# Kernel optimization log

Hardware: AMD Instinct MI355X
Metric: run time of the kernel (lower is better)

The kernel has to match this reference:

```python
import jax, jax.numpy as jnp
import numpy as np

T, B, D_IN, H = 512, 256, 64, 128


def _normc(key, shape):
    w = jax.random.normal(key, shape, dtype=jnp.float32)
    return w / jnp.sqrt(jnp.sum(w * w, axis=1, keepdims=True))


def setup_inputs() -> dict:
    key = jax.random.key(0)
    ks = jax.random.split(key, 8)
    state = jax.random.normal(ks[0], (T, B, D_IN), dtype=jnp.float32)
    # PyTorch LSTMCell params: weight_ih [4H, in], weight_hh [4H, H], biases [4H]
    s = 1.0 / np.sqrt(H)
    W_ih0 = jax.random.uniform(ks[1], (4 * H, D_IN), minval=-s, maxval=s, dtype=jnp.float32)
    W_hh0 = jax.random.uniform(ks[2], (4 * H, H), minval=-s, maxval=s, dtype=jnp.float32)
    b_ih0 = jnp.zeros((4 * H,), jnp.float32)
    b_hh0 = jnp.zeros((4 * H,), jnp.float32)
    W_ih1 = jax.random.uniform(ks[3], (4 * H, H), minval=-s, maxval=s, dtype=jnp.float32)
    W_hh1 = jax.random.uniform(ks[4], (4 * H, H), minval=-s, maxval=s, dtype=jnp.float32)
    b_ih1 = jnp.zeros((4 * H,), jnp.float32)
    b_hh1 = jnp.zeros((4 * H,), jnp.float32)
    # normc-initialized output head (rows normalized to unit norm, zero bias)
    W_out = _normc(ks[5], (1, H))
    b_out = jnp.zeros((1,), jnp.float32)
    return dict(state=state, W_ih0=W_ih0, W_hh0=W_hh0, b_ih0=b_ih0, b_hh0=b_hh0,
                W_ih1=W_ih1, W_hh1=W_hh1, b_ih1=b_ih1, b_hh1=b_hh1,
                W_out=W_out, b_out=b_out)


def _lstm_cell(x, h, c, W_ih, W_hh, b_ih, b_hh):
    # gates: [B, 4H], chunk order i, f, g, o (PyTorch convention)
    g = x @ W_ih.T + b_ih + h @ W_hh.T + b_hh
    i, f, gg, o = jnp.split(g, 4, axis=-1)
    i = jax.nn.sigmoid(i)
    f = jax.nn.sigmoid(f)
    gg = jnp.tanh(gg)
    o = jax.nn.sigmoid(o)
    c2 = f * c + i * gg
    h2 = o * jnp.tanh(c2)
    return h2, c2


def reference(state, W_ih0, W_hh0, b_ih0, b_hh0, W_ih1, W_hh1, b_ih1, b_hh1, W_out, b_out):
    Bsz = state.shape[1]
    Hd = W_hh0.shape[1]
    z = jnp.zeros((Bsz, Hd), state.dtype)

    def step(carry, x_t):
        h0, c0, h1, c1 = carry
        h0, c0 = _lstm_cell(x_t, h0, c0, W_ih0, W_hh0, b_ih0, b_hh0)
        h1, c1 = _lstm_cell(h0, h1, c1, W_ih1, W_hh1, b_ih1, b_hh1)
        v_t = h1 @ W_out.T + b_out  # [B, 1]
        return (h0, c0, h1, c1), v_t

    _, values = jax.lax.scan(step, (z, z, z, z), state)
    return values  # [T, B, 1]
```

## Files before the change

kernel.cpp:

```cpp
#include <hip/hip_runtime.h>


#define T_STEPS 512
#define BATCH   256
#define DIN     64
#define GROUP   16
#define NGRP    (T_STEPS / GROUP)

typedef _Float16 half8 __attribute__((ext_vector_type(8)));
typedef _Float16 half4 __attribute__((ext_vector_type(4)));
typedef float    f32x4 __attribute__((ext_vector_type(4)));

#define LOG2E  1.44269504088896f
#define LOG2E2 2.88539008177793f

#define WH_IH0 0
#define WH_HH0 32768
#define WH_IH1 98304
#define WH_HH1 163840
#define WH_X2     229376
#define WH_SLAB2  8617984
#define WB_FLAG2  50790400
#define WS2_TOTAL 50823168
#define WH_SLAB1  229376
#define WB_FLAG1  34013184
#define WS1_TOTAL 34045952
#define WS0XH_TOTAL ((size_t)(WH_X2 + 8388608) * 2)

__global__ void prep_weights(const float* __restrict__ wih0,
                             const float* __restrict__ whh0,
                             const float* __restrict__ wih1,
                             const float* __restrict__ whh1,
                             _Float16* __restrict__ ws) {
    int idx = blockIdx.x * 256 + threadIdx.x;
    float v; int row;
    if (idx < 32768)       { row = idx >> 6;             v = wih0[idx]; }
    else if (idx < 98304)  { row = (idx - 32768) >> 7;   v = whh0[idx - 32768]; }
    else if (idx < 163840) { row = (idx - 98304) >> 7;   v = wih1[idx - 98304]; }
    else                   { row = (idx - 163840) >> 7;  v = whh1[idx - 163840]; }
    float sc = ((row >> 7) == 2) ? LOG2E2 : LOG2E;
    ws[idx] = (_Float16)(v * sc);
}

__global__ void prep_state(const float* __restrict__ s, _Float16* __restrict__ d) {
    int i = (blockIdx.x * 256 + threadIdx.x) * 8;
    f32x4 a = *(const f32x4*)(s + i);
    f32x4 b = *(const f32x4*)(s + i + 4);
    half8 h;
    h[0]=(_Float16)a[0]; h[1]=(_Float16)a[1]; h[2]=(_Float16)a[2]; h[3]=(_Float16)a[3];
    h[4]=(_Float16)b[0]; h[5]=(_Float16)b[1]; h[6]=(_Float16)b[2]; h[7]=(_Float16)b[3];
    *(half8*)(d + i) = h;
}

__device__ __forceinline__ float rcpf(float x) { return __builtin_amdgcn_rcpf(x); }
__device__ __forceinline__ float ex2(float x)  { return __builtin_amdgcn_exp2f(x); }

__device__ __forceinline__ float sig2(float y) {
    return rcpf(1.0f + ex2(-y));
}
__device__ __forceinline__ float tanh2(float y2) {
    return 1.0f - 2.0f * rcpf(1.0f + ex2(y2));
}
__device__ __forceinline__ float tanh_c(float c) {
    return 1.0f - 2.0f * rcpf(1.0f + ex2(c * LOG2E2));
}

__device__ __forceinline__ float act_row(float aI, float aF, float aG, float aO,
                                         float& ccv) {
    float Ei = ex2(-aI);
    float Ef = ex2(-aF);
    float Eg = ex2(aG);
    float Eo = ex2(-aO);
    float fg  = rcpf(1.0f + Ef);
    float igg = (Eg - 1.0f) * rcpf((1.0f + Ei) * (1.0f + Eg));
    float c   = fg * ccv + igg;
    ccv = c;
    float Ec = ex2(c * LOG2E2);
    return (Ec - 1.0f) * rcpf((1.0f + Eo) * (1.0f + Ec));
}

#define PIPE_LDS_BYTES ((4096 + 128) * 2)

template<bool XH>
__global__ __launch_bounds__(512, 1) void lstm_pipe(
        const float* __restrict__ state32, const _Float16* __restrict__ wsw,
        const float* __restrict__ b_ih0, const float* __restrict__ b_hh0,
        const float* __restrict__ b_ih1, const float* __restrict__ b_hh1,
        const float* __restrict__ w_out, const float* __restrict__ b_out,
        _Float16* __restrict__ slab, int* __restrict__ flags,
        const _Float16* __restrict__ xh, float* __restrict__ out) {
    extern __shared__ _Float16 lds[];
    _Float16* hdb   = lds;
    _Float16* woutl = lds + 4096;

    const int tid  = threadIdx.x;
    const int w    = tid >> 6;
    const int lane = tid & 63;
    const int col  = lane & 15;
    const int quad = lane >> 4;
    const bool producer = blockIdx.x < 16;
    const int tile = blockIdx.x & 15;
    const int rowbase = tile * 16;
    const int j0 = w * 16 + col;

    {
        half8 z;
        #pragma unroll
        for (int jj = 0; jj < 8; ++jj) z[jj] = (_Float16)0.0f;
        *(half8*)(hdb + tid * 8) = z;
    }
    if (!producer && tid < 128) woutl[tid] = (_Float16)w_out[tid];

    half8 wresf[4][4];
    float bias[4];
    #pragma unroll
    for (int nt = 0; nt < 4; ++nt) {
        int j = nt * 128 + j0;
        float sc = (nt == 2) ? LOG2E2 : LOG2E;
        if (producer) {
            #pragma unroll
            for (int kt = 0; kt < 2; ++kt)
                wresf[nt][kt] = *(const half8*)(wsw + WH_IH0 + j * 64 + kt * 32 + quad * 8);
            bias[nt] = (b_ih0[j] + b_hh0[j]) * sc;
        } else {
            #pragma unroll
            for (int kt = 0; kt < 4; ++kt)
                wresf[nt][kt] = *(const half8*)(wsw + WH_IH1 + j * 128 + kt * 32 + quad * 8);
            bias[nt] = (b_ih1[j] + b_hh1[j]) * sc;
        }
    }
    const float bout = b_out[0];

    half8 wpf[4][4];
    {
        const _Float16* wrg = wsw + (producer ? WH_HH0 : WH_HH1);
        #pragma unroll
        for (int kt = 0; kt < 4; ++kt)
            #pragma unroll
            for (int nt = 0; nt < 4; ++nt)
                wpf[kt][nt] = *(const half8*)(wrg + (nt * 128 + j0) * 128 + kt * 32 + quad * 8);
    }
    #pragma unroll
    for (int kt = 0; kt < 4; ++kt)
        #pragma unroll
        for (int nt = 0; nt < 4; ++nt)
            asm volatile("" : "+v"(wpf[kt][nt]));

    int swz[4], hoff[4], w0off[4];
    #pragma unroll
    for (int kt = 0; kt < 4; ++kt) {
        swz[kt]  = ((kt * 4 + quad) ^ col) * 8;
        hoff[kt] = col * 128 + swz[kt];
    }
    #pragma unroll
    for (int i = 0; i < 4; ++i) {
        int row = quad * 4 + i;
        w0off[i] = row * 128 + (((2 * w + (col >> 3)) ^ row) * 8) + (col & 7);
    }
    float cc[4] = {0.f, 0.f, 0.f, 0.f};

    const int cr   = tid >> 5;
    const int cc0  = (tid & 31) * 4;
    const int cprd = cr * 128 + (((cc0 >> 3) ^ cr) * 8) + (cc0 & 7);

    __syncthreads();

    if (producer) {
        const _Float16* xph = xh + (size_t)(rowbase + col) * DIN + quad * 8;
        const float*    xpf = state32 + (size_t)(rowbase + col) * DIN + quad * 8;

        half8 bx0, bx1;
        f32x4 bf0, bf1, bf2, bf3;
        f32x4 accI[4];
        {
            half8 a0, a1v;
            if constexpr (XH) {
                a0  = *(const half8*)(xph);
                a1v = *(const half8*)(xph + 32);
            } else {
                f32x4 t0 = *(const f32x4*)(xpf),      t1 = *(const f32x4*)(xpf + 4);
                f32x4 t2 = *(const f32x4*)(xpf + 32), t3 = *(const f32x4*)(xpf + 36);
                #pragma unroll
                for (int jj = 0; jj < 4; ++jj) {
                    a0[jj]  = (_Float16)t0[jj]; a0[jj+4]  = (_Float16)t1[jj];
                    a1v[jj] = (_Float16)t2[jj]; a1v[jj+4] = (_Float16)t3[jj];
                }
            }
            #pragma unroll
            for (int nt = 0; nt < 4; ++nt) {
                f32x4 b = {bias[nt], bias[nt], bias[nt], bias[nt]};
                accI[nt] = b;
            }
            #pragma unroll
            for (int nt = 0; nt < 4; ++nt)
                accI[nt] = __builtin_amdgcn_mfma_f32_16x16x32_f16(a0, wresf[nt][0], accI[nt], 0, 0, 0);
            #pragma unroll
            for (int nt = 0; nt < 4; ++nt)
                accI[nt] = __builtin_amdgcn_mfma_f32_16x16x32_f16(a1v, wresf[nt][1], accI[nt], 0, 0, 0);
            if constexpr (XH) {
                bx0 = *(const half8*)(xph + BATCH * DIN);
                bx1 = *(const half8*)(xph + BATCH * DIN + 32);
            } else {
                bf0 = *(const f32x4*)(xpf + BATCH * DIN);
                bf1 = *(const f32x4*)(xpf + BATCH * DIN + 4);
                bf2 = *(const f32x4*)(xpf + BATCH * DIN + 32);
                bf3 = *(const f32x4*)(xpf + BATCH * DIN + 36);
            }
        }

        #pragma unroll 2
        for (int t = 0; t < T_STEPS; ++t) {
            const int pbo = (t & 1) * 2048, cbo = pbo ^ 2048;
            const int lt = t & (GROUP - 1);
            __syncthreads();

            if (t > 0) {
                half4 hv = *(const half4*)(hdb + pbo + cprd);
                *(half4*)(slab + (size_t)((t - 1) * 16 + tile) * 2048 + tid * 4) = hv;
            }
            if (lt == 1 && t > 16 && tid == 0)
                __hip_atomic_store(flags + ((t >> 4) - 1) * 16 + tile, t >> 4,
                                   __ATOMIC_RELEASE, __HIP_MEMORY_SCOPE_AGENT);

            half8 ah[4];
            #pragma unroll
            for (int kt = 0; kt < 4; ++kt)
                ah[kt] = *(const half8*)(hdb + pbo + hoff[kt]);

            #pragma unroll
            for (int kt = 0; kt < 4; ++kt)
                #pragma unroll
                for (int nt = 0; nt < 4; ++nt)
                    accI[nt] = __builtin_amdgcn_mfma_f32_16x16x32_f16(ah[kt], wpf[kt][nt], accI[nt], 0, 0, 0);

            half8 fx0, fx1;
            f32x4 ff0, ff1, ff2, ff3;
            {
                int tn2 = (t + 2 < T_STEPS) ? t + 2 : T_STEPS - 1;
                if constexpr (XH) {
                    const _Float16* xq = xph + (size_t)tn2 * (BATCH * DIN);
                    fx0 = *(const half8*)(xq);
                    fx1 = *(const half8*)(xq + 32);
                } else {
                    const float* xq = xpf + (size_t)tn2 * (BATCH * DIN);
                    ff0 = *(const f32x4*)(xq);      ff1 = *(const f32x4*)(xq + 4);
                    ff2 = *(const f32x4*)(xq + 32); ff3 = *(const f32x4*)(xq + 36);
                }
            }

            half8 cx0, cx1;
            if constexpr (XH) { cx0 = bx0; cx1 = bx1; }
            else {
                #pragma unroll
                for (int jj = 0; jj < 4; ++jj) {
                    cx0[jj] = (_Float16)bf0[jj]; cx0[jj+4] = (_Float16)bf1[jj];
                    cx1[jj] = (_Float16)bf2[jj]; cx1[jj+4] = (_Float16)bf3[jj];
                }
            }
            f32x4 accN[4];
            #pragma unroll
            for (int nt = 0; nt < 4; ++nt) {
                f32x4 b = {bias[nt], bias[nt], bias[nt], bias[nt]};
                accN[nt] = b;
            }
            #pragma unroll
            for (int i = 0; i < 4; ++i) {
                if (i < 2) {
                    half8 cxk = (i == 0) ? cx0 : cx1;
                    #pragma unroll
                    for (int nt = 0; nt < 4; ++nt)
                        accN[nt] = __builtin_amdgcn_mfma_f32_16x16x32_f16(cxk, wresf[nt][i], accN[nt], 0, 0, 0);
                    __builtin_amdgcn_sched_group_barrier(0x008, 4, 0);
                }
                float hval = act_row(accI[0][i], accI[1][i], accI[2][i], accI[3][i], cc[i]);
                hdb[cbo + w0off[i]] = (_Float16)hval;
                __builtin_amdgcn_sched_group_barrier(0x002, 16, 0);
            }

            #pragma unroll
            for (int nt = 0; nt < 4; ++nt) accI[nt] = accN[nt];
            if constexpr (XH) { bx0 = fx0; bx1 = fx1; }
            else { bf0 = ff0; bf1 = ff1; bf2 = ff2; bf3 = ff3; }
        }
        __syncthreads();
        {
            half4 hv = *(const half4*)(hdb + 0 + cprd);
            *(half4*)(slab + (size_t)((T_STEPS - 1) * 16 + tile) * 2048 + tid * 4) = hv;
        }
        __syncthreads();
        if (tid == 0)
            __hip_atomic_store(flags + (NGRP - 1) * 16 + tile, NGRP,
                               __ATOMIC_RELEASE, __HIP_MEMORY_SCOPE_AGENT);
    } else {
        if (tid == 0) {
            while (__hip_atomic_load(flags + tile, __ATOMIC_ACQUIRE,
                                     __HIP_MEMORY_SCOPE_AGENT) < 1)
                __builtin_amdgcn_s_sleep(1);
        }
        __syncthreads();

        half8 uA[4];
        f32x4 accI[4];
        {
            const _Float16* s0 = slab + (size_t)tile * 2048;
            half8 cA[4];
            #pragma unroll
            for (int kt = 0; kt < 4; ++kt)
                cA[kt] = *(const half8*)(s0 + col * 128 + kt * 32 + quad * 8);
            #pragma unroll
            for (int nt = 0; nt < 4; ++nt) {
                f32x4 b = {bias[nt], bias[nt], bias[nt], bias[nt]};
                accI[nt] = b;
            }
            #pragma unroll
            for (int kt = 0; kt < 4; ++kt)
                #pragma unroll
                for (int nt = 0; nt < 4; ++nt)
                    accI[nt] = __builtin_amdgcn_mfma_f32_16x16x32_f16(cA[kt], wresf[nt][kt], accI[nt], 0, 0, 0);
            const _Float16* s1 = slab + (size_t)(16 + tile) * 2048;
            #pragma unroll
            for (int kt = 0; kt < 4; ++kt)
                uA[kt] = *(const half8*)(s1 + col * 128 + kt * 32 + quad * 8);
        }

        #pragma unroll 2
        for (int t = 0; t < T_STEPS; ++t) {
            const int pbo = (t & 1) * 2048, cbo = pbo ^ 2048;
            const int lt = t & (GROUP - 1);
            __syncthreads();

            half8 a1[4];
            #pragma unroll
            for (int kt = 0; kt < 4; ++kt)
                a1[kt] = *(const half8*)(hdb + pbo + hoff[kt]);

            #pragma unroll
            for (int kt = 0; kt < 4; ++kt)
                #pragma unroll
                for (int nt = 0; nt < 4; ++nt)
                    accI[nt] = __builtin_amdgcn_mfma_f32_16x16x32_f16(a1[kt], wpf[kt][nt], accI[nt], 0, 0, 0);

            if (lt == 12 && tid == 0) {
                int g1 = (t >> 4) + 1;
                if (g1 < NGRP) {
                    while (__hip_atomic_load(flags + g1 * 16 + tile, __ATOMIC_ACQUIRE,
                                             __HIP_MEMORY_SCOPE_AGENT) < g1 + 1)
                        __builtin_amdgcn_s_sleep(1);
                }
            }

            half8 fA[4];
            {
                int tn2 = (t + 2 < T_STEPS) ? t + 2 : T_STEPS - 1;
                const _Float16* sq = slab + (size_t)(tn2 * 16 + tile) * 2048;
                #pragma unroll
                for (int kt = 0; kt < 4; ++kt)
                    fA[kt] = *(const half8*)(sq + col * 128 + kt * 32 + quad * 8);
            }

            f32x4 accN[4];
            #pragma unroll
            for (int nt = 0; nt < 4; ++nt) {
                f32x4 b = {bias[nt], bias[nt], bias[nt], bias[nt]};
                accN[nt] = b;
            }
            #pragma unroll
            for (int i = 0; i < 4; ++i) {
                #pragma unroll
                for (int nt = 0; nt < 4; ++nt)
                    accN[nt] = __builtin_amdgcn_mfma_f32_16x16x32_f16(uA[i], wresf[nt][i], accN[nt], 0, 0, 0);
                __builtin_amdgcn_sched_group_barrier(0x008, 4, 0);
                float hval = act_row(accI[0][i], accI[1][i], accI[2][i], accI[3][i], cc[i]);
                hdb[cbo + w0off[i]] = (_Float16)hval;
                __builtin_amdgcn_sched_group_barrier(0x002, 16, 0);
            }

            if (w == 7) {
                f32x4 vh = {0.f, 0.f, 0.f, 0.f};
                #pragma unroll
                for (int kt = 0; kt < 4; ++kt) {
                    half8 av = *(const half8*)(hdb + pbo + hoff[kt]);
                    half8 bw = *(const half8*)(woutl + kt * 32 + quad * 8);
                    vh = __builtin_amdgcn_mfma_f32_16x16x32_f16(av, bw, vh, 0, 0, 0);
                }
                if (t > 0 && col == 0) {
                    f32x4 vo = {vh[0] + bout, vh[1] + bout, vh[2] + bout, vh[3] + bout};
                    *(f32x4*)(out + (size_t)(t - 1) * BATCH + rowbase + quad * 4) = vo;
                }
            }

            #pragma unroll
            for (int nt = 0; nt < 4; ++nt) accI[nt] = accN[nt];
            #pragma unroll
            for (int kt = 0; kt < 4; ++kt) uA[kt] = fA[kt];
        }
        __syncthreads();
        if (w == 7) {
            const int fbo = (((T_STEPS - 1) & 1) ^ 1) * 2048;
            f32x4 vh = {0.f, 0.f, 0.f, 0.f};
            #pragma unroll
            for (int kt = 0; kt < 4; ++kt) {
                half8 av = *(const half8*)(hdb + fbo + hoff[kt]);
                half8 bw = *(const half8*)(woutl + kt * 32 + quad * 8);
                vh = __builtin_amdgcn_mfma_f32_16x16x32_f16(av, bw, vh, 0, 0, 0);
            }
            if (col == 0) {
                f32x4 vo = {vh[0] + bout, vh[1] + bout, vh[2] + bout, vh[3] + bout};
                *(f32x4*)(out + (size_t)(T_STEPS - 1) * BATCH + rowbase + quad * 4) = vo;
            }
        }
    }
}

#define MONO_LDS_BYTES ((73728 + 128) * 2)

template<bool XH>
__global__ __launch_bounds__(512, 2) void lstm_mono(
        const float* __restrict__ state32, const _Float16* __restrict__ wsw,
        const float* __restrict__ b_ih0, const float* __restrict__ b_hh0,
        const float* __restrict__ b_ih1, const float* __restrict__ b_hh1,
        const float* __restrict__ w_out, const float* __restrict__ b_out,
        float* __restrict__ out) {
    extern __shared__ _Float16 lds[];
    _Float16* whh1  = lds;
    _Float16* h0b   = lds + 65536;
    _Float16* h1b   = lds + 69632;
    _Float16* woutl = lds + 73728;

    const int tid  = threadIdx.x;
    const int w    = tid >> 6;
    const int lane = tid & 63;
    const int col  = lane & 15;
    const int quad = lane >> 4;
    const int rowbase = blockIdx.x * 16;
    const int j0 = w * 16 + col;

    const _Float16* whh1g = wsw + WH_HH1;
    #pragma unroll
    for (int it = 0; it < 16; ++it) {
        int flat = (it * 512 + tid) * 8;
        int r = flat >> 7, chunk = (flat >> 3) & 15;
        *(half8*)(whh1 + r * 128 + ((chunk ^ (r & 15)) * 8)) = *(const half8*)(whh1g + flat);
    }
    {
        half8 z;
        #pragma unroll
        for (int jj = 0; jj < 8; ++jj) z[jj] = (_Float16)0.0f;
        for (int i = tid * 8; i < 8192; i += 4096) *(half8*)(h0b + i) = z;
    }
    if (tid < 128) woutl[tid] = (_Float16)w_out[tid];

    half8 whh0f[4][4], wih1f[4][4];
    float bias0[4], bias1[4];
    #pragma unroll
    for (int nt = 0; nt < 4; ++nt) {
        int j = nt * 128 + j0;
        float sc = (nt == 2) ? LOG2E2 : LOG2E;
        #pragma unroll
        for (int kt = 0; kt < 4; ++kt) {
            whh0f[nt][kt] = *(const half8*)(wsw + WH_HH0 + j * 128 + kt * 32 + quad * 8);
            wih1f[nt][kt] = *(const half8*)(wsw + WH_IH1 + j * 128 + kt * 32 + quad * 8);
        }
        bias0[nt] = (b_ih0[j] + b_hh0[j]) * sc;
        bias1[nt] = (b_ih1[j] + b_hh1[j]) * sc;
    }
    const float bout = b_out[0];

    int swz[4], hoff[4], w0off[4];
    #pragma unroll
    for (int kt = 0; kt < 4; ++kt) {
        swz[kt]  = ((kt * 4 + quad) ^ col) * 8;
        hoff[kt] = col * 128 + swz[kt];
    }
    #pragma unroll
    for (int i = 0; i < 4; ++i) {
        int row = quad * 4 + i;
        w0off[i] = row * 128 + (((2 * w + (col >> 3)) ^ row) * 8) + (col & 7);
    }
    float c0[4] = {0.f,0.f,0.f,0.f}, c1[4] = {0.f,0.f,0.f,0.f};

    const _Float16* xph = wsw + WH_X2 + (size_t)(rowbase + col) * DIN + quad * 8;
    const float*    xpf = state32 + (size_t)(rowbase + col) * DIN + quad * 8;
    half8 nxh0, nxh1;
    f32x4 nxf0, nxf1, nxf2, nxf3;
    if constexpr (XH) {
        nxh0 = *(const half8*)(xph); nxh1 = *(const half8*)(xph + 32);
    } else {
        nxf0 = *(const f32x4*)(xpf);      nxf1 = *(const f32x4*)(xpf + 4);
        nxf2 = *(const f32x4*)(xpf + 32); nxf3 = *(const f32x4*)(xpf + 36);
    }
    __syncthreads();
    const _Float16* wih0g = wsw + WH_IH0;

    #pragma unroll 1
    for (int t = 0; t < T_STEPS; ++t) {
        const int pbo = (t & 1) * 2048, cbo = pbo ^ 2048;
        half8 ax0, ax1;
        if constexpr (XH) { ax0 = nxh0; ax1 = nxh1; }
        else {
            #pragma unroll
            for (int jj = 0; jj < 4; ++jj) {
                ax0[jj]   = (_Float16)nxf0[jj]; ax0[jj+4] = (_Float16)nxf1[jj];
                ax1[jj]   = (_Float16)nxf2[jj]; ax1[jj+4] = (_Float16)nxf3[jj];
            }
        }
        half8 wif[4][2];
        #pragma unroll
        for (int nt = 0; nt < 4; ++nt)
            #pragma unroll
            for (int kt = 0; kt < 2; ++kt)
                wif[nt][kt] = *(const half8*)(wih0g + (nt * 128 + j0) * 64 + kt * 32 + quad * 8);
        half8 ah[4];
        #pragma unroll
        for (int kt = 0; kt < 4; ++kt)
            ah[kt] = *(const half8*)(h0b + pbo + hoff[kt]);

        f32x4 acc[4];
        #pragma unroll
        for (int nt = 0; nt < 4; ++nt) {
            f32x4 b = {bias0[nt], bias0[nt], bias0[nt], bias0[nt]};
            acc[nt] = b;
        }
        #pragma unroll
        for (int kt = 0; kt < 4; ++kt)
            #pragma unroll
            for (int nt = 0; nt < 4; ++nt)
                acc[nt] = __builtin_amdgcn_mfma_f32_16x16x32_f16(ah[kt], whh0f[nt][kt], acc[nt], 0, 0, 0);
        #pragma unroll
        for (int kt = 0; kt < 2; ++kt) {
            half8 axk = kt ? ax1 : ax0;
            #pragma unroll
            for (int nt = 0; nt < 4; ++nt)
                acc[nt] = __builtin_amdgcn_mfma_f32_16x16x32_f16(axk, wif[nt][kt], acc[nt], 0, 0, 0);
        }
        {
            int tn = (t + 1 < T_STEPS) ? t + 1 : t;
            if constexpr (XH) {
                const _Float16* xq = xph + (size_t)tn * (BATCH * DIN);
                nxh0 = *(const half8*)(xq); nxh1 = *(const half8*)(xq + 32);
            } else {
                const float* xq = xpf + (size_t)tn * (BATCH * DIN);
                nxf0 = *(const f32x4*)(xq);      nxf1 = *(const f32x4*)(xq + 4);
                nxf2 = *(const f32x4*)(xq + 32); nxf3 = *(const f32x4*)(xq + 36);
            }
        }
        #pragma unroll
        for (int i = 0; i < 4; ++i) {
            float ig = sig2(acc[0][i]);
            float fg = sig2(acc[1][i]);
            float gg = tanh2(acc[2][i]);
            float og = sig2(acc[3][i]);
            float c  = fg * c0[i] + ig * gg;
            c0[i] = c;
            h0b[cbo + w0off[i]] = (_Float16)(og * tanh_c(c));
        }
        __syncthreads();

        #pragma unroll
        for (int nt = 0; nt < 4; ++nt) {
            f32x4 b = {bias1[nt], bias1[nt], bias1[nt], bias1[nt]};
            acc[nt] = b;
        }
        #pragma unroll
        for (int kt = 0; kt < 4; ++kt) {
            half8 a0 = *(const half8*)(h0b + cbo + hoff[kt]);
            half8 a1 = *(const half8*)(h1b + pbo + hoff[kt]);
            #pragma unroll
            for (int nt = 0; nt < 4; ++nt)
                acc[nt] = __builtin_amdgcn_mfma_f32_16x16x32_f16(a0, wih1f[nt][kt], acc[nt], 0, 0, 0);
            #pragma unroll
            for (int nt = 0; nt < 4; ++nt) {
                half8 bfr = *(const half8*)(whh1 + nt * 16384 + j0 * 128 + swz[kt]);
                acc[nt] = __builtin_amdgcn_mfma_f32_16x16x32_f16(a1, bfr, acc[nt], 0, 0, 0);
            }
        }
        #pragma unroll
        for (int i = 0; i < 4; ++i) {
            float ig = sig2(acc[0][i]);
            float fg = sig2(acc[1][i]);
            float gg = tanh2(acc[2][i]);
            float og = sig2(acc[3][i]);
            float c  = fg * c1[i] + ig * gg;
            c1[i] = c;
            h1b[cbo + w0off[i]] = (_Float16)(og * tanh_c(c));
        }
        if (w == 7) {
            f32x4 vh = {0.f, 0.f, 0.f, 0.f};
            #pragma unroll
            for (int kt = 0; kt < 4; ++kt) {
                half8 a1 = *(const half8*)(h1b + pbo + hoff[kt]);
                half8 bw = *(const half8*)(woutl + kt * 32 + quad * 8);
                vh = __builtin_amdgcn_mfma_f32_16x16x32_f16(a1, bw, vh, 0, 0, 0);
            }
            if (t > 0 && col == 0) {
                f32x4 vo = {vh[0] + bout, vh[1] + bout, vh[2] + bout, vh[3] + bout};
                *(f32x4*)(out + (size_t)(t - 1) * BATCH + rowbase + quad * 4) = vo;
            }
        }
    }
    __syncthreads();
    if (w == 7) {
        const int fbo = (((T_STEPS - 1) & 1) ^ 1) * 2048;
        f32x4 vh = {0.f, 0.f, 0.f, 0.f};
        #pragma unroll
        for (int kt = 0; kt < 4; ++kt) {
            half8 a1 = *(const half8*)(h1b + fbo + hoff[kt]);
            half8 bw = *(const half8*)(woutl + kt * 32 + quad * 8);
            vh = __builtin_amdgcn_mfma_f32_16x16x32_f16(a1, bw, vh, 0, 0, 0);
        }
        if (col == 0) {
            f32x4 vo = {vh[0] + bout, vh[1] + bout, vh[2] + bout, vh[3] + bout};
            *(f32x4*)(out + (size_t)(T_STEPS - 1) * BATCH + rowbase + quad * 4) = vo;
        }
    }
}

extern "C" void kernel_launch(void* const* d_in, const int* in_sizes, int n_in,
                              void* d_out, int out_size, void* d_ws, size_t ws_size,
                              hipStream_t stream) {
    const float* state = (const float*)d_in[0];
    const float* wih0  = (const float*)d_in[1];
    const float* whh0  = (const float*)d_in[2];
    const float* bih0  = (const float*)d_in[3];
    const float* bhh0  = (const float*)d_in[4];
    const float* wih1  = (const float*)d_in[5];
    const float* whh1  = (const float*)d_in[6];
    const float* bih1  = (const float*)d_in[7];
    const float* bhh1  = (const float*)d_in[8];
    const float* wout  = (const float*)d_in[9];
    const float* bout  = (const float*)d_in[10];
    _Float16* wsh = (_Float16*)d_ws;
    float* outp = (float*)d_out;

    prep_weights<<<896, 256, 0, stream>>>(wih0, whh0, wih1, whh1, wsh);

    if (ws_size >= WS2_TOTAL) {
        prep_state<<<4096, 256, 0, stream>>>(state, wsh + WH_X2);
        lstm_pipe<true><<<32, 512, PIPE_LDS_BYTES, stream>>>(
            state, wsh, bih0, bhh0, bih1, bhh1, wout, bout,
            wsh + WH_SLAB2, (int*)((char*)d_ws + WB_FLAG2), wsh + WH_X2, outp);
    } else if (ws_size >= WS1_TOTAL) {
        lstm_pipe<false><<<32, 512, PIPE_LDS_BYTES, stream>>>(
            state, wsh, bih0, bhh0, bih1, bhh1, wout, bout,
            wsh + WH_SLAB1, (int*)((char*)d_ws + WB_FLAG1), nullptr, outp);
    } else if (ws_size >= WS0XH_TOTAL) {
        prep_state<<<4096, 256, 0, stream>>>(state, wsh + WH_X2);
        lstm_mono<true><<<16, 512, MONO_LDS_BYTES, stream>>>(
            state, wsh, bih0, bhh0, bih1, bhh1, wout, bout, outp);
    } else {
        lstm_mono<false><<<16, 512, MONO_LDS_BYTES, stream>>>(
            state, wsh, bih0, bhh0, bih1, bhh1, wout, bout, outp);
    }
}
```

Measured before the change: 608.7 us.

## Drop fp16 state pre-conversion pass and fold bias into first MFMA

Removes the separate prep_state kernel and the fp16 copy of the input sequence, so the pipelined LSTM always reads fp32 state and converts it in-register. This skips an extra kernel launch and a full pass over the 32 MB input, at the cost of twice the bytes read per step inside the recurrent loop. Bias is now passed as the accumulator operand of the first MFMA instead of being splatted separately. The explicit sched_group_barrier interleaving of MFMA and activation code is also removed, leaving instruction scheduling to the compiler.

```diff
diff --git a/kernel.cpp b/kernel.cpp
--- a/kernel.cpp
+++ b/kernel.cpp
@@ -18,14 +18,9 @@
 #define WH_HH0 32768
 #define WH_IH1 98304
 #define WH_HH1 163840
-#define WH_X2     229376
-#define WH_SLAB2  8617984
-#define WB_FLAG2  50790400
-#define WS2_TOTAL 50823168
 #define WH_SLAB1  229376
 #define WB_FLAG1  34013184
 #define WS1_TOTAL 34045952
-#define WS0XH_TOTAL ((size_t)(WH_X2 + 8388608) * 2)
 
 __global__ void prep_weights(const float* __restrict__ wih0,
                              const float* __restrict__ whh0,
@@ -42,28 +37,12 @@
     ws[idx] = (_Float16)(v * sc);
 }
 
-__global__ void prep_state(const float* __restrict__ s, _Float16* __restrict__ d) {
-    int i = (blockIdx.x * 256 + threadIdx.x) * 8;
-    f32x4 a = *(const f32x4*)(s + i);
-    f32x4 b = *(const f32x4*)(s + i + 4);
-    half8 h;
-    h[0]=(_Float16)a[0]; h[1]=(_Float16)a[1]; h[2]=(_Float16)a[2]; h[3]=(_Float16)a[3];
-    h[4]=(_Float16)b[0]; h[5]=(_Float16)b[1]; h[6]=(_Float16)b[2]; h[7]=(_Float16)b[3];
-    *(half8*)(d + i) = h;
-}
-
 __device__ __forceinline__ float rcpf(float x) { return __builtin_amdgcn_rcpf(x); }
 __device__ __forceinline__ float ex2(float x)  { return __builtin_amdgcn_exp2f(x); }
 
-__device__ __forceinline__ float sig2(float y) {
-    return rcpf(1.0f + ex2(-y));
-}
-__device__ __forceinline__ float tanh2(float y2) {
-    return 1.0f - 2.0f * rcpf(1.0f + ex2(y2));
-}
-__device__ __forceinline__ float tanh_c(float c) {
-    return 1.0f - 2.0f * rcpf(1.0f + ex2(c * LOG2E2));
-}
+__device__ __forceinline__ float sig2(float y)  { return rcpf(1.0f + ex2(-y)); }
+__device__ __forceinline__ float tanh2(float y2){ return 1.0f - 2.0f * rcpf(1.0f + ex2(y2)); }
+__device__ __forceinline__ float tanh_c(float c){ return 1.0f - 2.0f * rcpf(1.0f + ex2(c * LOG2E2)); }
 
 __device__ __forceinline__ float act_row(float aI, float aF, float aG, float aO,
                                          float& ccv) {
@@ -81,14 +60,13 @@
 
 #define PIPE_LDS_BYTES ((4096 + 128) * 2)
 
-template<bool XH>
 __global__ __launch_bounds__(512, 1) void lstm_pipe(
         const float* __restrict__ state32, const _Float16* __restrict__ wsw,
         const float* __restrict__ b_ih0, const float* __restrict__ b_hh0,
         const float* __restrict__ b_ih1, const float* __restrict__ b_hh1,
         const float* __restrict__ w_out, const float* __restrict__ b_out,
         _Float16* __restrict__ slab, int* __restrict__ flags,
-        const _Float16* __restrict__ xh, float* __restrict__ out) {
+        float* __restrict__ out) {
     extern __shared__ _Float16 lds[];
     _Float16* hdb   = lds;
     _Float16* woutl = lds + 4096;
@@ -112,22 +90,25 @@
     if (!producer && tid < 128) woutl[tid] = (_Float16)w_out[tid];
 
     half8 wresf[4][4];
-    float bias[4];
+    f32x4 biasv[4];
     #pragma unroll
     for (int nt = 0; nt < 4; ++nt) {
         int j = nt * 128 + j0;
         float sc = (nt == 2) ? LOG2E2 : LOG2E;
+        float b;
         if (producer) {
             #pragma unroll
             for (int kt = 0; kt < 2; ++kt)
                 wresf[nt][kt] = *(const half8*)(wsw + WH_IH0 + j * 64 + kt * 32 + quad * 8);
-            bias[nt] = (b_ih0[j] + b_hh0[j]) * sc;
+            b = (b_ih0[j] + b_hh0[j]) * sc;
         } else {
             #pragma unroll
             for (int kt = 0; kt < 4; ++kt)
                 wresf[nt][kt] = *(const half8*)(wsw + WH_IH1 + j * 128 + kt * 32 + quad * 8);
-            bias[nt] = (b_ih1[j] + b_hh1[j]) * sc;
-        }
+            b = (b_ih1[j] + b_hh1[j]) * sc;
+        }
+        f32x4 bv = {b, b, b, b};
+        biasv[nt] = bv;
     }
     const float bout = b_out[0];
 
@@ -166,46 +147,29 @@
     __syncthreads();
 
     if (producer) {
-        const _Float16* xph = xh + (size_t)(rowbase + col) * DIN + quad * 8;
-        const float*    xpf = state32 + (size_t)(rowbase + col) * DIN + quad * 8;
-
-        half8 bx0, bx1;
+        const float* xpf = state32 + (size_t)(rowbase + col) * DIN + quad * 8;
+
         f32x4 bf0, bf1, bf2, bf3;
         f32x4 accI[4];
         {
+            f32x4 t0 = *(const f32x4*)(xpf),      t1 = *(const f32x4*)(xpf + 4);
+            f32x4 t2 = *(const f32x4*)(xpf + 32), t3 = *(const f32x4*)(xpf + 36);
             half8 a0, a1v;
-            if constexpr (XH) {
-                a0  = *(const half8*)(xph);
-                a1v = *(const half8*)(xph + 32);
-            } else {
-                f32x4 t0 = *(const f32x4*)(xpf),      t1 = *(const f32x4*)(xpf + 4);
-                f32x4 t2 = *(const f32x4*)(xpf + 32), t3 = *(const f32x4*)(xpf + 36);
-                #pragma unroll
-                for (int jj = 0; jj < 4; ++jj) {
-                    a0[jj]  = (_Float16)t0[jj]; a0[jj+4]  = (_Float16)t1[jj];
-                    a1v[jj] = (_Float16)t2[jj]; a1v[jj+4] = (_Float16)t3[jj];
-                }
-            }
-            #pragma unroll
-            for (int nt = 0; nt < 4; ++nt) {
-                f32x4 b = {bias[nt], bias[nt], bias[nt], bias[nt]};
-                accI[nt] = b;
-            }
-            #pragma unroll
-            for (int nt = 0; nt < 4; ++nt)
-                accI[nt] = __builtin_amdgcn_mfma_f32_16x16x32_f16(a0, wresf[nt][0], accI[nt], 0, 0, 0);
+            #pragma unroll
+            for (int jj = 0; jj < 4; ++jj) {
+                a0[jj]  = (_Float16)t0[jj]; a0[jj+4]  = (_Float16)t1[jj];
+                a1v[jj] = (_Float16)t2[jj]; a1v[jj+4] = (_Float16)t3[jj];
+            }
+            #pragma unroll
+            for (int nt = 0; nt < 4; ++nt)
+                accI[nt] = __builtin_amdgcn_mfma_f32_16x16x32_f16(a0, wresf[nt][0], biasv[nt], 0, 0, 0);
             #pragma unroll
             for (int nt = 0; nt < 4; ++nt)
                 accI[nt] = __builtin_amdgcn_mfma_f32_16x16x32_f16(a1v, wresf[nt][1], accI[nt], 0, 0, 0);
-            if constexpr (XH) {
-                bx0 = *(const half8*)(xph + BATCH * DIN);
-                bx1 = *(const half8*)(xph + BATCH * DIN + 32);
-            } else {
-                bf0 = *(const f32x4*)(xpf + BATCH * DIN);
-                bf1 = *(const f32x4*)(xpf + BATCH * DIN + 4);
-                bf2 = *(const f32x4*)(xpf + BATCH * DIN + 32);
-                bf3 = *(const f32x4*)(xpf + BATCH * DIN + 36);
-            }
+            bf0 = *(const f32x4*)(xpf + BATCH * DIN);
+            bf1 = *(const f32x4*)(xpf + BATCH * DIN + 4);
+            bf2 = *(const f32x4*)(xpf + BATCH * DIN + 32);
+            bf3 = *(const f32x4*)(xpf + BATCH * DIN + 36);
         }
 
         #pragma unroll 2
@@ -233,54 +197,37 @@
                 for (int nt = 0; nt < 4; ++nt)
                     accI[nt] = __builtin_amdgcn_mfma_f32_16x16x32_f16(ah[kt], wpf[kt][nt], accI[nt], 0, 0, 0);
 
-            half8 fx0, fx1;
             f32x4 ff0, ff1, ff2, ff3;
             {
                 int tn2 = (t + 2 < T_STEPS) ? t + 2 : T_STEPS - 1;
-                if constexpr (XH) {
-                    const _Float16* xq = xph + (size_t)tn2 * (BATCH * DIN);
-                    fx0 = *(const half8*)(xq);
-                    fx1 = *(const half8*)(xq + 32);
-                } else {
-                    const float* xq = xpf + (size_t)tn2 * (BATCH * DIN);
-                    ff0 = *(const f32x4*)(xq);      ff1 = *(const f32x4*)(xq + 4);
-                    ff2 = *(const f32x4*)(xq + 32); ff3 = *(const f32x4*)(xq + 36);
-                }
+                const float* xq = xpf + (size_t)tn2 * (BATCH * DIN);
+                ff0 = *(const f32x4*)(xq);      ff1 = *(const f32x4*)(xq + 4);
+                ff2 = *(const f32x4*)(xq + 32); ff3 = *(const f32x4*)(xq + 36);
             }
 
             half8 cx0, cx1;
-            if constexpr (XH) { cx0 = bx0; cx1 = bx1; }
-            else {
-                #pragma unroll
-                for (int jj = 0; jj < 4; ++jj) {
-                    cx0[jj] = (_Float16)bf0[jj]; cx0[jj+4] = (_Float16)bf1[jj];
-                    cx1[jj] = (_Float16)bf2[jj]; cx1[jj+4] = (_Float16)bf3[jj];
-                }
+            #pragma unroll
+            for (int jj = 0; jj < 4; ++jj) {
+                cx0[jj] = (_Float16)bf0[jj]; cx0[jj+4] = (_Float16)bf1[jj];
+                cx1[jj] = (_Float16)bf2[jj]; cx1[jj+4] = (_Float16)bf3[jj];
             }
             f32x4 accN[4];
             #pragma unroll
-            for (int nt = 0; nt < 4; ++nt) {
-                f32x4 b = {bias[nt], bias[nt], bias[nt], bias[nt]};
-                accN[nt] = b;
-            }
+            for (int nt = 0; nt < 4; ++nt)
+                accN[nt] = __builtin_amdgcn_mfma_f32_16x16x32_f16(cx0, wresf[nt][0], biasv[nt], 0, 0, 0);
+            #pragma unroll
+            for (int nt = 0; nt < 4; ++nt)
+                accN[nt] = __builtin_amdgcn_mfma_f32_16x16x32_f16(cx1, wresf[nt][1], accN[nt], 0, 0, 0);
+
             #pragma unroll
             for (int i = 0; i < 4; ++i) {
-                if (i < 2) {
-                    half8 cxk = (i == 0) ? cx0 : cx1;
-                    #pragma unroll
-                    for (int nt = 0; nt < 4; ++nt)
-                        accN[nt] = __builtin_amdgcn_mfma_f32_16x16x32_f16(cxk, wresf[nt][i], accN[nt], 0, 0, 0);
-                    __builtin_amdgcn_sched_group_barrier(0x008, 4, 0);
-                }
                 float hval = act_row(accI[0][i], accI[1][i], accI[2][i], accI[3][i], cc[i]);
                 hdb[cbo + w0off[i]] = (_Float16)hval;
-                __builtin_amdgcn_sched_group_barrier(0x002, 16, 0);
             }
 
             #pragma unroll
             for (int nt = 0; nt < 4; ++nt) accI[nt] = accN[nt];
-            if constexpr (XH) { bx0 = fx0; bx1 = fx1; }
-            else { bf0 = ff0; bf1 = ff1; bf2 = ff2; bf3 = ff3; }
+            bf0 = ff0; bf1 = ff1; bf2 = ff2; bf3 = ff3;
         }
         __syncthreads();
         {
@@ -308,12 +255,10 @@
             for (int kt = 0; kt < 4; ++kt)
                 cA[kt] = *(const half8*)(s0 + col * 128 + kt * 32 + quad * 8);
             #pragma unroll
-            for (int nt = 0; nt < 4; ++nt) {
-                f32x4 b = {bias[nt], bias[nt], bias[nt], bias[nt]};
-                accI[nt] = b;
-            }
-            #pragma unroll
-            for (int kt = 0; kt < 4; ++kt)
+            for (int nt = 0; nt < 4; ++nt)
+                accI[nt] = __builtin_amdgcn_mfma_f32_16x16x32_f16(cA[0], wresf[nt][0], biasv[nt], 0, 0, 0);
+            #pragma unroll
+            for (int kt = 1; kt < 4; ++kt)
                 #pragma unroll
                 for (int nt = 0; nt < 4; ++nt)
                     accI[nt] = __builtin_amdgcn_mfma_f32_16x16x32_f16(cA[kt], wresf[nt][kt], accI[nt], 0, 0, 0);
@@ -360,19 +305,18 @@
 
             f32x4 accN[4];
             #pragma unroll
-            for (int nt = 0; nt < 4; ++nt) {
-                f32x4 b = {bias[nt], bias[nt], bias[nt], bias[nt]};
-                accN[nt] = b;
-            }
-            #pragma unroll
-            for (int i = 0; i < 4; ++i) {
+            for (int nt = 0; nt < 4; ++nt)
+                accN[nt] = __builtin_amdgcn_mfma_f32_16x16x32_f16(uA[0], wresf[nt][0], biasv[nt], 0, 0, 0);
+            #pragma unroll
+            for (int kt = 1; kt < 4; ++kt)
                 #pragma unroll
                 for (int nt = 0; nt < 4; ++nt)
-                    accN[nt] = __builtin_amdgcn_mfma_f32_16x16x32_f16(uA[i], wresf[nt][i], accN[nt], 0, 0, 0);
-                __builtin_amdgcn_sched_group_barrier(0x008, 4, 0);
+                    accN[nt] = __builtin_amdgcn_mfma_f32_16x16x32_f16(uA[kt], wresf[nt][kt], accN[nt], 0, 0, 0);
+
+            #pragma unroll
+            for (int i = 0; i < 4; ++i) {
                 float hval = act_row(accI[0][i], accI[1][i], accI[2][i], accI[3][i], cc[i]);
                 hdb[cbo + w0off[i]] = (_Float16)hval;
-                __builtin_amdgcn_sched_group_barrier(0x002, 16, 0);
             }
 
             if (w == 7) {
@@ -414,7 +358,6 @@
 
 #define MONO_LDS_BYTES ((73728 + 128) * 2)
 
-template<bool XH>
 __global__ __launch_bounds__(512, 2) void lstm_mono(
         const float* __restrict__ state32, const _Float16* __restrict__ wsw,
         const float* __restrict__ b_ih0, const float* __restrict__ b_hh0,
@@ -479,16 +422,9 @@
     }
     float c0[4] = {0.f,0.f,0.f,0.f}, c1[4] = {0.f,0.f,0.f,0.f};
 
-    const _Float16* xph = wsw + WH_X2 + (size_t)(rowbase + col) * DIN + quad * 8;
-    const float*    xpf = state32 + (size_t)(rowbase + col) * DIN + quad * 8;
-    half8 nxh0, nxh1;
-    f32x4 nxf0, nxf1, nxf2, nxf3;
-    if constexpr (XH) {
-        nxh0 = *(const half8*)(xph); nxh1 = *(const half8*)(xph + 32);
-    } else {
-        nxf0 = *(const f32x4*)(xpf);      nxf1 = *(const f32x4*)(xpf + 4);
-        nxf2 = *(const f32x4*)(xpf + 32); nxf3 = *(const f32x4*)(xpf + 36);
-    }
+    const float* xpf = state32 + (size_t)(rowbase + col) * DIN + quad * 8;
+    f32x4 nxf0 = *(const f32x4*)(xpf),      nxf1 = *(const f32x4*)(xpf + 4);
+    f32x4 nxf2 = *(const f32x4*)(xpf + 32), nxf3 = *(const f32x4*)(xpf + 36);
     __syncthreads();
     const _Float16* wih0g = wsw + WH_IH0;
 
@@ -496,13 +432,10 @@
     for (int t = 0; t < T_STEPS; ++t) {
         const int pbo = (t & 1) * 2048, cbo = pbo ^ 2048;
         half8 ax0, ax1;
-        if constexpr (XH) { ax0 = nxh0; ax1 = nxh1; }
-        else {
-            #pragma unroll
-            for (int jj = 0; jj < 4; ++jj) {
-                ax0[jj]   = (_Float16)nxf0[jj]; ax0[jj+4] = (_Float16)nxf1[jj];
-                ax1[jj]   = (_Float16)nxf2[jj]; ax1[jj+4] = (_Float16)nxf3[jj];
-            }
+        #pragma unroll
+        for (int jj = 0; jj < 4; ++jj) {
+            ax0[jj]   = (_Float16)nxf0[jj]; ax0[jj+4] = (_Float16)nxf1[jj];
+            ax1[jj]   = (_Float16)nxf2[jj]; ax1[jj+4] = (_Float16)nxf3[jj];
         }
         half8 wif[4][2];
         #pragma unroll
@@ -535,14 +468,9 @@
         }
         {
             int tn = (t + 1 < T_STEPS) ? t + 1 : t;
-            if constexpr (XH) {
-                const _Float16* xq = xph + (size_t)tn * (BATCH * DIN);
-                nxh0 = *(const half8*)(xq); nxh1 = *(const half8*)(xq + 32);
-            } else {
-                const float* xq = xpf + (size_t)tn * (BATCH * DIN);
-                nxf0 = *(const f32x4*)(xq);      nxf1 = *(const f32x4*)(xq + 4);
-                nxf2 = *(const f32x4*)(xq + 32); nxf3 = *(const f32x4*)(xq + 36);
-            }
+            const float* xq = xpf + (size_t)tn * (BATCH * DIN);
+            nxf0 = *(const f32x4*)(xq);      nxf1 = *(const f32x4*)(xq + 4);
+            nxf2 = *(const f32x4*)(xq + 32); nxf3 = *(const f32x4*)(xq + 36);
         }
         #pragma unroll
         for (int i = 0; i < 4; ++i) {
@@ -634,21 +562,12 @@
 
     prep_weights<<<896, 256, 0, stream>>>(wih0, whh0, wih1, whh1, wsh);
 
-    if (ws_size >= WS2_TOTAL) {
-        prep_state<<<4096, 256, 0, stream>>>(state, wsh + WH_X2);
-        lstm_pipe<true><<<32, 512, PIPE_LDS_BYTES, stream>>>(
+    if (ws_size >= WS1_TOTAL) {
+        lstm_pipe<<<32, 512, PIPE_LDS_BYTES, stream>>>(
             state, wsh, bih0, bhh0, bih1, bhh1, wout, bout,
-            wsh + WH_SLAB2, (int*)((char*)d_ws + WB_FLAG2), wsh + WH_X2, outp);
-    } else if (ws_size >= WS1_TOTAL) {
-        lstm_pipe<false><<<32, 512, PIPE_LDS_BYTES, stream>>>(
-            state, wsh, bih0, bhh0, bih1, bhh1, wout, bout,
-            wsh + WH_SLAB1, (int*)((char*)d_ws + WB_FLAG1), nullptr, outp);
-    } else if (ws_size >= WS0XH_TOTAL) {
-        prep_state<<<4096, 256, 0, stream>>>(state, wsh + WH_X2);
-        lstm_mono<true><<<16, 512, MONO_LDS_BYTES, stream>>>(
+            wsh + WH_SLAB1, (int*)((char*)d_ws + WB_FLAG1), outp);
+    } else {
+        lstm_mono<<<16, 512, MONO_LDS_BYTES, stream>>>(
             state, wsh, bih0, bhh0, bih1, bhh1, wout, bout, outp);
-    } else {
-        lstm_mono<false><<<16, 512, MONO_LDS_BYTES, stream>>>(
-            state, wsh, bih0, bhh0, bih1, bhh1, wout, bout, outp);
     }
 }
```

Result: slower. 646.9 us (+6.3%).
